# Kernel optimization log

Hardware: AMD Instinct MI355X
Metric: run time of the kernel (lower is better)

## Reference

```python
import jax, jax.numpy as jnp
import numpy as np

# dims: batch, seq_len, d_model, heads, head_dim, n_buckets
B, L, DM, H, DH, K = 4, 4096, 1024, 16, 64, 8
C = L // K            # chunk length after bucket sort (512); extra_len==0 for these dims
CS = 0.1              # cluster_score mixing weight


def setup_inputs() -> dict:
    key = jax.random.key(0)
    ks = jax.random.split(key, 12)
    s = 0.02
    def p(k, shape):
        return jax.random.normal(k, shape, jnp.float32) * s
    return {
        "inputs_q": jax.random.normal(ks[0], (B, L, DM), jnp.float32),
        "wq": p(ks[1], (DM, H, DH)), "bq": jnp.zeros((H, DH), jnp.float32),
        "wk": p(ks[2], (DM, H, DH)), "bk": jnp.zeros((H, DH), jnp.float32),
        "wv": p(ks[3], (DM, H, DH)), "bv": jnp.zeros((H, DH), jnp.float32),
        "w_shared": p(ks[4], (H, DH, K)),
        "w_qscore": p(ks[5], (H, DH, K)),
        "w_kscore": p(ks[6], (H, DH, K)),
        "wo": p(ks[7], (H, DH, DM)), "bo": jnp.zeros((DM,), jnp.float32),
    }


def reference(inputs_q, wq, bq, wk, bk, wv, bv, w_shared, w_qscore, w_kscore, wo, bo):
    scale = 1.0 / np.sqrt(DH)
    # QKV projections (DenseGeneral to (H, DH))
    q = jnp.einsum('bld,dhk->blhk', inputs_q, wq) + bq  # [B,L,H,DH]
    k = jnp.einsum('bld,dhk->blhk', inputs_q, wk) + bk
    v = jnp.einsum('bld,dhk->blhk', inputs_q, wv) + bv

    # learned linear cluster scores on stop-gradient q/k
    mix_q = (1.0 - CS) * w_shared + CS * w_qscore  # [H,DH,K]
    mix_k = (1.0 - CS) * w_shared + CS * w_kscore
    qs = jnp.einsum('blhd,hdk->blhk', jax.lax.stop_gradient(q), mix_q)  # [B,L,H,K]
    ksc = jnp.einsum('blhd,hdk->blhk', jax.lax.stop_gradient(k), mix_k)

    # bucket assignment = argmax learned score; per-(batch,head) stable sort by bucket id
    bq_id = jnp.argmax(qs, -1).transpose(0, 2, 1)   # [B,H,L]
    bk_id = jnp.argmax(ksc, -1).transpose(0, 2, 1)
    sort_q = jnp.argsort(bq_id, axis=-1)            # stable in jax
    sort_k = jnp.argsort(bk_id, axis=-1)

    qh = q.transpose(0, 2, 1, 3)  # [B,H,L,DH]
    kh = k.transpose(0, 2, 1, 3)
    vh = v.transpose(0, 2, 1, 3)
    sq = jnp.take_along_axis(qh, sort_q[..., None], axis=2).reshape(B, H, K, C, DH)
    sk = jnp.take_along_axis(kh, sort_k[..., None], axis=2).reshape(B, H, K, C, DH)
    sv = jnp.take_along_axis(vh, sort_k[..., None], axis=2).reshape(B, H, K, C, DH)

    # block attention within each bucket chunk
    logits = jnp.einsum('bhncd,bhned->bhnce', sq, sk) * scale  # [B,H,K,C,C]
    attn = jax.nn.softmax(logits, axis=-1)
    o = jnp.einsum('bhnce,bhned->bhncd', attn, sv).reshape(B, H, L, DH)

    # unsort back to original token order
    inv_q = jnp.argsort(sort_q, axis=-1)
    o = jnp.take_along_axis(o, inv_q[..., None], axis=2)  # [B,H,L,DH]
    o = o.transpose(0, 2, 1, 3)                            # [B,L,H,DH]

    out = jnp.einsum('blhd,hdo->blo', o, wo) + bo          # output projection

    # auxiliary load-balancing routing loss over buckets (extra_loss)
    p_q = jax.nn.softmax(qs, -1)
    p_k = jax.nn.softmax(ksc, -1)
    f_q = jax.nn.one_hot(jnp.argmax(qs, -1), K, dtype=qs.dtype)
    f_k = jax.nn.one_hot(jnp.argmax(ksc, -1), K, dtype=qs.dtype)
    lq = K * jnp.mean(jnp.sum(jnp.mean(f_q, 1) * jnp.mean(p_q, 1), -1))
    lk = K * jnp.mean(jnp.sum(jnp.mean(f_k, 1) * jnp.mean(p_k, 1), -1))
    extra_loss = 0.5 * (lq + lk)
    return out, extra_loss
```

## Files before the change

### kernel.cpp

```cpp
#include <hip/hip_runtime.h>
#include <hip/hip_bf16.h>

#define BB 4
#define LL 4096
#define DM 1024
#define HH 16
#define DHD 64
#define KB 8
#define BL 16384
#define FLAGCAP 131072

typedef __attribute__((ext_vector_type(8))) short short8;
typedef __attribute__((ext_vector_type(4))) short short4v;
typedef __attribute__((ext_vector_type(4))) float float4v;

#define MFMA16(A, Bx, C) __builtin_amdgcn_mfma_f32_16x16x32_bf16(A, Bx, C, 0, 0, 0)

static __device__ __forceinline__ short bf16s(float f) {
  __hip_bfloat16 h = __float2bfloat16(f);
  return *reinterpret_cast<short*>(&h);
}
static __device__ __forceinline__ float b2f(short s) {
  __hip_bfloat16 h = *reinterpret_cast<__hip_bfloat16*>(&s);
  return __bfloat162float(h);
}
static __device__ __forceinline__ void gl16(const void* g, void* l) {
  __builtin_amdgcn_global_load_lds(
      (const __attribute__((address_space(1))) void*)g,
      (__attribute__((address_space(3))) void*)l, 16, 0, 0);
}

__global__ __launch_bounds__(256) void prep_wt(const float* __restrict__ wq,
                                               const float* __restrict__ wk,
                                               const float* __restrict__ wv,
                                               const float* __restrict__ wo,
                                               __hip_bfloat16* __restrict__ wt_qkv,
                                               __hip_bfloat16* __restrict__ wt_o) {
  int blk = blockIdx.x;
  int s = blk >> 8;
  int rem = blk & 255;
  int k0 = (rem >> 4) * 64;
  int n0 = (rem & 15) * 64;
  const float* src = (s == 0) ? wq : (s == 1) ? wk : (s == 2) ? wv : wo;
  __hip_bfloat16* dst = (s < 3) ? (wt_qkv + (size_t)s * 1024 * 1024) : wt_o;
  __shared__ float ls[64][65];
  int t = threadIdx.x;
#pragma unroll
  for (int p = 0; p < 4; ++p) {
    int sid = p * 256 + t;
    int r = sid >> 4, c4 = sid & 15;
    float4 v = *reinterpret_cast<const float4*>(src + (size_t)(k0 + r) * 1024 + n0 + c4 * 4);
    ls[r][c4 * 4 + 0] = v.x; ls[r][c4 * 4 + 1] = v.y;
    ls[r][c4 * 4 + 2] = v.z; ls[r][c4 * 4 + 3] = v.w;
  }
  __syncthreads();
#pragma unroll
  for (int p = 0; p < 4; ++p) {
    int sid = p * 256 + t;
    int n = sid >> 4, kq = sid & 15;
    short4v pk;
#pragma unroll
    for (int j = 0; j < 4; ++j) pk[j] = bf16s(ls[kq * 4 + j][n]);
    *reinterpret_cast<short4v*>(dst + (size_t)(n0 + n) * 1024 + k0 + kq * 4) = pk;
  }
}

__global__ __launch_bounds__(256) void prep_wsc(const float* __restrict__ wq,
                                                const float* __restrict__ wk,
                                                const float* __restrict__ wsh,
                                                const float* __restrict__ wqs,
                                                const float* __restrict__ wks,
                                                const float* __restrict__ bq,
                                                const float* __restrict__ bk,
                                                double* __restrict__ wscg,
                                                double* __restrict__ bsc,
                                                __hip_bfloat16* __restrict__ whb,
                                                __hip_bfloat16* __restrict__ wmb) {
  int col = blockIdx.x;
  int side = col >> 7, h = (col >> 3) & 15, kk = col & 7;
  int g = side * 16 + h;
  const float* w = side ? wk : wq;
  const float* wscore = side ? wks : wqs;
  __shared__ double mix[64];
  int t = threadIdx.x;
  if (t < 64)
    mix[t] = 0.9 * (double)wsh[(h * 64 + t) * 8 + kk] +
             0.1 * (double)wscore[(h * 64 + t) * 8 + kk];
  __syncthreads();
#pragma unroll
  for (int p = 0; p < 4; ++p) {
    int d = p * 256 + t;
    double acc = 0.0;
    const float* wr = w + (size_t)d * 1024 + h * 64;
#pragma unroll
    for (int j = 0; j < 64; ++j) acc += (double)wr[j] * mix[j];
    wscg[((size_t)g * 1024 + d) * 8 + kk] = acc;
    short hi = bf16s((float)acc);
    short mid = bf16s((float)(acc - (double)b2f(hi)));
    *reinterpret_cast<short*>(whb + (size_t)col * 1024 + d) = hi;
    *reinterpret_cast<short*>(wmb + (size_t)col * 1024 + d) = mid;
  }
  if (t == 0) {
    const float* br = (side ? bk : bq) + h * 64;
    double acc = 0.0;
    for (int j = 0; j < 64; ++j) acc += (double)br[j] * mix[j];
    bsc[col] = acc;
  }
}

__global__ __launch_bounds__(256) void score_gemm(const float* __restrict__ x,
                                                  const __hip_bfloat16* __restrict__ whb,
                                                  const __hip_bfloat16* __restrict__ wmb,
                                                  const double* __restrict__ bsc,
                                                  __hip_bfloat16* __restrict__ xb,
                                                  int* __restrict__ bid,
                                                  float* __restrict__ psumg,
                                                  int* __restrict__ flagcnt,
                                                  int* __restrict__ list) {
  __shared__ char sm[81920];
  int t = threadIdx.x;
  int m0 = blockIdx.x * 64;
  int n0 = blockIdx.y * 128;
  int lane = t & 63;
  int wu = __builtin_amdgcn_readfirstlane(t >> 6);
  int lm = lane & 15, quad = lane >> 4;
  int wmr = (wu & 1) * 32, wn = (wu >> 1) * 64;
  int rb = wu * 32, rr = lane >> 3, phys = lane & 7;

  auto STAGEB = [&](int bufsel, int k0) {
    char* base = sm + 16384 + bufsel * 32768;
#pragma unroll
    for (int p = 0; p < 4; ++p) {
      int row = rb + p * 8 + rr;
      int kc = (phys - row) & 7;
      gl16(whb + (size_t)(n0 + row) * 1024 + k0 + kc * 8, base + (rb + p * 8) * 128);
      gl16(wmb + (size_t)(n0 + row) * 1024 + k0 + kc * 8, base + 16384 + (rb + p * 8) * 128);
    }
  };

  float4 xf[2][2];
  auto LOADX = [&](int k0) {
#pragma unroll
    for (int p = 0; p < 2; ++p) {
      int sid = p * 256 + t;
      int m = sid >> 3, kc = sid & 7;
      const float* ap = x + (size_t)(m0 + m) * 1024 + k0 + kc * 8;
      xf[p][0] = *reinterpret_cast<const float4*>(ap);
      xf[p][1] = *reinterpret_cast<const float4*>(ap + 4);
    }
  };

  STAGEB(0, 0);
  LOADX(0);

  float4v zero = {0.f, 0.f, 0.f, 0.f};
  float4v acc[2][4];
#pragma unroll
  for (int i = 0; i < 2; ++i)
#pragma unroll
    for (int j = 0; j < 4; ++j) acc[i][j] = zero;

#pragma unroll 1
  for (int kt = 0; kt < 16; ++kt) {
    int k0 = kt * 64;
    short8 hi[2], lo[2];
#pragma unroll
    for (int p = 0; p < 2; ++p) {
      float vv[8] = {xf[p][0].x, xf[p][0].y, xf[p][0].z, xf[p][0].w,
                     xf[p][1].x, xf[p][1].y, xf[p][1].z, xf[p][1].w};
#pragma unroll
      for (int e = 0; e < 8; ++e) {
        short h = bf16s(vv[e]);
        hi[p][e] = h;
        lo[p][e] = bf16s(vv[e] - b2f(h));
      }
    }
    asm volatile("" ::: "memory");
    __builtin_amdgcn_s_barrier();
    asm volatile("" ::: "memory");
#pragma unroll
    for (int p = 0; p < 2; ++p) {
      int sid = p * 256 + t;
      int m = sid >> 3, kc = sid & 7;
      *reinterpret_cast<short8*>(sm + m * 128 + ((kc + m) & 7) * 16) = hi[p];
      *reinterpret_cast<short8*>(sm + 8192 + m * 128 + ((kc + m) & 7) * 16) = lo[p];
      if (blockIdx.y == 0)
        *reinterpret_cast<short8*>(xb + (size_t)(m0 + m) * 1024 + k0 + kc * 8) = hi[p];
    }
    if (kt < 15) {
      STAGEB((kt + 1) & 1, k0 + 64);
      LOADX(k0 + 64);
      asm volatile("s_waitcnt vmcnt(12)" ::: "memory");
    } else {
      asm volatile("s_waitcnt vmcnt(0)" ::: "memory");
    }
    asm volatile("s_waitcnt lgkmcnt(0)" ::: "memory");
    __builtin_amdgcn_s_barrier();
    asm volatile("" ::: "memory");

    const char* bb = sm + 16384 + (kt & 1) * 32768;
#pragma unroll
    for (int kh = 0; kh < 2; ++kh) {
      short8 ah[2], al[2], bh[4], bm[4];
#pragma unroll
      for (int i = 0; i < 2; ++i) {
        int row = wmr + i * 16 + lm;
        int ph = ((kh * 4 + quad) + row) & 7;
        ah[i] = *reinterpret_cast<const short8*>(sm + row * 128 + ph * 16);
        al[i] = *reinterpret_cast<const short8*>(sm + 8192 + row * 128 + ph * 16);
      }
#pragma unroll
      for (int j = 0; j < 4; ++j) {
        int rn = wn + j * 16 + lm;
        int ph = ((kh * 4 + quad) + rn) & 7;
        bh[j] = *reinterpret_cast<const short8*>(bb + rn * 128 + ph * 16);
        bm[j] = *reinterpret_cast<const short8*>(bb + 16384 + rn * 128 + ph * 16);
      }
#pragma unroll
      for (int i = 0; i < 2; ++i)
#pragma unroll
        for (int j = 0; j < 4; ++j) {
          acc[i][j] = MFMA16(ah[i], bh[j], acc[i][j]);
          acc[i][j] = MFMA16(ah[i], bm[j], acc[i][j]);
          acc[i][j] = MFMA16(al[i], bh[j], acc[i][j]);
        }
    }
  }

  int b = m0 >> 12;
  int l0 = m0 & 4095;
  int kk = lm & 7;
#pragma unroll
  for (int j = 0; j < 4; ++j) {
    int n = n0 + wn + j * 16 + lm;
    int g = n >> 3;
    int side = g >> 4, h = g & 15;
    int slab = (side * 4 + b) * 16 + h;
    float bias = (float)bsc[n];
    float pp = 0.f;
#pragma unroll
    for (int i = 0; i < 2; ++i)
#pragma unroll
      for (int r = 0; r < 4; ++r) {
        float v = acc[i][j][r] + bias;
        float bmx = v; int bi = kk;
#pragma unroll
        for (int o = 1; o < 8; o <<= 1) {
          float vo = __shfl_xor(bmx, o);
          int io = __shfl_xor(bi, o);
          if (vo > bmx || (vo == bmx && io < bi)) { bmx = vo; bi = io; }
        }
        float vm = (kk == bi) ? -3.0e38f : v;
#pragma unroll
        for (int o = 1; o < 8; o <<= 1) vm = fmaxf(vm, __shfl_xor(vm, o));
        float e = __expf(v - bmx);
        float es = e;
#pragma unroll
        for (int o = 1; o < 8; o <<= 1) es += __shfl_xor(es, o);
        pp += e * (1.f / es);
        int l = l0 + wmr + i * 16 + quad * 4 + r;
        if (kk == 0) {
          bid[(slab << 12) | l] = bi;
          if (bmx - vm < 5e-4f) {
            int pos = atomicAdd(flagcnt, 1);
            if (pos < FLAGCAP) list[pos] = (slab << 12) | l;
          }
        }
      }
    pp += __shfl_xor(pp, 16);
    pp += __shfl_xor(pp, 32);
    if (quad == 0) atomicAdd(&psumg[slab * 8 + kk], pp);
  }
}

__global__ __launch_bounds__(256) void refine_kernel(const float* __restrict__ x,
                                                     const double* __restrict__ wscg,
                                                     const double* __restrict__ bsc,
                                                     const int* __restrict__ flagcnt,
                                                     const int* __restrict__ list,
                                                     int* __restrict__ bid) {
  int lane = threadIdx.x & 63;
  int w = threadIdx.x >> 6;
  int cnt = flagcnt[0];
  if (cnt > FLAGCAP) cnt = FLAGCAP;
  for (int i = blockIdx.x * 4 + w; i < cnt; i += 1024) {
    int e = list[i];
    int slab = e >> 12, l = e & 4095;
    int side = slab >> 6, b = (slab >> 4) & 3, h = slab & 15;
    int g = side * 16 + h;
    int row = b * 4096 + l;
    double acc[8] = {0, 0, 0, 0, 0, 0, 0, 0};
    const float* xr = x + (size_t)row * 1024 + lane * 16;
    const double* wr = wscg + ((size_t)g * 1024 + lane * 16) * 8;
#pragma unroll
    for (int dd = 0; dd < 16; ++dd) {
      double xv = (double)xr[dd];
#pragma unroll
      for (int j = 0; j < 8; ++j) acc[j] += xv * wr[dd * 8 + j];
    }
#pragma unroll
    for (int j = 0; j < 8; ++j) {
      double v = acc[j];
      v += __shfl_xor(v, 32); v += __shfl_xor(v, 16); v += __shfl_xor(v, 8);
      v += __shfl_xor(v, 4);  v += __shfl_xor(v, 2);  v += __shfl_xor(v, 1);
      acc[j] = v + bsc[g * 8 + j];
    }
    if (lane == 0) {
      double mx = acc[0]; int am = 0;
#pragma unroll
      for (int j = 1; j < 8; ++j) { if (acc[j] > mx) { mx = acc[j]; am = j; } }
      bid[(slab << 12) | l] = am;
    }
  }
}

__global__ __launch_bounds__(256) void sort_kernel(const int* __restrict__ bid,
                                                   int* __restrict__ sortq,
                                                   int* __restrict__ sortk,
                                                   int* __restrict__ cntg) {
  int blk = blockIdx.x;
  int side = blk >> 6, b = (blk >> 4) & 3, h = blk & 15;
  const int* ids = bid + (((side * 4 + b) * 16 + h) << 12);
  int* outp = (side ? sortk : sortq) + ((b * 16 + h) << 12);
  __shared__ int cnt[8][257];
  __shared__ int base[8];
  int t = threadIdx.x;
  int loc[16];
  int hist[8] = {0, 0, 0, 0, 0, 0, 0, 0};
#pragma unroll
  for (int j = 0; j < 16; ++j) { loc[j] = ids[t * 16 + j] & 7; hist[loc[j]]++; }
#pragma unroll
  for (int k = 0; k < 8; ++k) cnt[k][t + 1] = hist[k];
  if (t < 8) cnt[t][0] = 0;
  __syncthreads();
  if (t < 8) {
    for (int i = 1; i <= 256; ++i) cnt[t][i] += cnt[t][i - 1];
  }
  __syncthreads();
  if (t == 0) {
    int run = 0;
    for (int k = 0; k < 8; ++k) { base[k] = run; run += cnt[k][256]; }
  }
  if (t < 8) cntg[((side * 4 + b) * 16 + h) * 8 + t] = cnt[t][256];
  __syncthreads();
#pragma unroll
  for (int j = 0; j < 16; ++j) {
    int k = loc[j];
    int before = 0;
#pragma unroll
    for (int i = 0; i < 16; ++i) before += (i < j && loc[i] == k) ? 1 : 0;
    int pos = base[k] + cnt[k][t] + before;
    outp[pos] = t * 16 + j;
  }
}

template <bool CBF16>
__global__ __launch_bounds__(512, 2) void gemm256(const __hip_bfloat16* __restrict__ A,
                                                  const __hip_bfloat16* __restrict__ Bt,
                                                  void* __restrict__ Cv,
                                                  const float* __restrict__ b0,
                                                  const float* __restrict__ b1,
                                                  const float* __restrict__ b2,
                                                  int nblk, int cpx) {
  __shared__ char sm[131072];
  int t = threadIdx.x;
  int blk = (blockIdx.x & 7) * cpx + (blockIdx.x >> 3);
  int m0 = (blk / nblk) * 256;
  int n0 = (blk % nblk) * 256;
  int lane = t & 63;
  int wu = __builtin_amdgcn_readfirstlane(t >> 6);
  int lm = lane & 15, quad = lane >> 4;
  int rr = lane >> 3, phys = lane & 7;
  int wrow = (wu & 1) * 64;
  int wcol = (wu >> 1) * 32;

  constexpr int QM[4] = {0, 0, 1, 1};
  constexpr int QN[4] = {0, 1, 1, 0};

  auto STAGE = [&](char* bufn, int j, int kS) {
    const int mat = (j == 1 || j == 2) ? 1 : 0;
    const int hm = (j >= 2) ? 1 : 0;
    const __hip_bfloat16* src = mat ? Bt : A;
    int gb = mat ? n0 : m0;
    char* lb = bufn + mat * 32768 + hm * 16384;
#pragma unroll
    for (int i = 0; i < 2; ++i) {
      int r = hm * 128 + (wu * 2 + i) * 8 + rr;
      int kc = (phys - r) & 7;
      gl16(src + (size_t)(gb + r) * 1024 + kS + kc * 8, lb + (wu * 2 + i) * 1024);
    }
  };

#pragma unroll
  for (int j = 0; j < 4; ++j) STAGE(sm, j, 0);

  float4v zero = {0.f, 0.f, 0.f, 0.f};
  float4v acc[4][4][2];
#pragma unroll
  for (int q = 0; q < 4; ++q)
#pragma unroll
    for (int mi = 0; mi < 4; ++mi)
#pragma unroll
      for (int ni = 0; ni < 2; ++ni) acc[q][mi][ni] = zero;

  short8 a[4][2], b[2][2];
  auto READA = [&](const char* bc, int qm) {
#pragma unroll
    for (int mi = 0; mi < 4; ++mi) {
      int row = qm * 128 + wrow + mi * 16 + lm;
#pragma unroll
      for (int ks = 0; ks < 2; ++ks) {
        int ph = ((ks * 4 + quad) + row) & 7;
        a[mi][ks] = *reinterpret_cast<const short8*>(bc + row * 128 + ph * 16);
      }
    }
  };
  auto READB = [&](const char* bc, int qn) {
#pragma unroll
    for (int ni = 0; ni < 2; ++ni) {
      int rn = qn * 128 + wcol + ni * 16 + lm;
#pragma unroll
      for (int ks = 0; ks < 2; ++ks) {
        int ph = ((ks * 4 + quad) + rn) & 7;
        b[ni][ks] = *reinterpret_cast<const short8*>(bc + 32768 + rn * 128 + ph * 16);
      }
    }
  };

#pragma unroll 1
  for (int kt = 0; kt < 16; ++kt) {
    char* bc = sm + ((kt & 1) << 16);
    char* bn = sm + (((kt & 1) ^ 1) << 16);
    int kS = (kt < 15) ? (kt + 1) * 64 : 960;
#pragma unroll
    for (int j = 0; j < 4; ++j) {
      if (j < 3) {
        asm volatile("s_waitcnt vmcnt(4)" ::: "memory");
        __builtin_amdgcn_s_barrier();
      }
      if (j == 0) { READA(bc, 0); READB(bc, 0); }
      else if (j == 1) { READB(bc, 1); }
      else if (j == 2) { READA(bc, 1); }
      else { READB(bc, 0); }
      STAGE(bn, j, kS);
      __builtin_amdgcn_s_setprio(1);
#pragma unroll
      for (int mi = 0; mi < 4; ++mi)
#pragma unroll
        for (int ni = 0; ni < 2; ++ni)
#pragma unroll
          for (int ks = 0; ks < 2; ++ks)
            acc[j][mi][ni] = MFMA16(a[mi][ks], b[ni][ks], acc[j][mi][ni]);
      __builtin_amdgcn_s_setprio(0);
    }
  }
  asm volatile("s_waitcnt vmcnt(0)" ::: "memory");

  if constexpr (CBF16) {
#pragma unroll
    for (int j = 0; j < 4; ++j)
#pragma unroll
      for (int mi = 0; mi < 4; ++mi)
#pragma unroll
        for (int ni = 0; ni < 2; ++ni) {
          int nn = n0 + QN[j] * 128 + wcol + ni * 16 + lm;
          int s = nn >> 10, nnb = nn & 1023;
          const float* bias = (s == 0) ? b0 : (s == 1) ? b1 : b2;
          float bvx = bias[nnb];
          __hip_bfloat16* C = (__hip_bfloat16*)Cv + (size_t)s * BL * 1024;
#pragma unroll
          for (int r = 0; r < 4; ++r) {
            int row = m0 + QM[j] * 128 + wrow + mi * 16 + quad * 4 + r;
            C[(size_t)row * 1024 + nnb] = __float2bfloat16(acc[j][mi][ni][r] + bvx);
          }
        }
  } else {
    float* C = (float*)Cv;
#pragma unroll
    for (int j = 0; j < 4; ++j)
#pragma unroll
      for (int mi = 0; mi < 4; ++mi)
#pragma unroll
        for (int ni = 0; ni < 2; ++ni) {
          int nn = n0 + QN[j] * 128 + wcol + ni * 16 + lm;
          float bvx = b0[nn];
#pragma unroll
          for (int r = 0; r < 4; ++r) {
            int row = m0 + QM[j] * 128 + wrow + mi * 16 + quad * 4 + r;
            C[(size_t)row * 1024 + nn] = acc[j][mi][ni][r] + bvx;
          }
        }
  }
}

__global__ __launch_bounds__(256) void vt_kernel(const __hip_bfloat16* __restrict__ vb,
                                                 const int* __restrict__ sortk,
                                                 __hip_bfloat16* __restrict__ vT) {
  int cid = blockIdx.x;
  int b = cid >> 7, h = (cid >> 3) & 15, n = cid & 7;
  int sbase = ((b * 16 + h) << 12) + n * 512;
  __shared__ __hip_bfloat16 ls[64][72];
  int t = threadIdx.x;
  for (int kt = 0; kt < 8; ++kt) {
    __syncthreads();
#pragma unroll
    for (int p = 0; p < 2; ++p) {
      int sid = p * 256 + t;
      int key = sid >> 3, kc = sid & 7;
      int tok = sortk[sbase + kt * 64 + key];
      short8 v = *reinterpret_cast<const short8*>(vb + ((size_t)(b * 4096 + tok) * 16 + h) * 64 + kc * 8);
      *reinterpret_cast<short8*>(&ls[key][kc * 8]) = v;
    }
    __syncthreads();
#pragma unroll
    for (int p = 0; p < 2; ++p) {
      int sid = p * 256 + t;
      int dim = sid >> 3, kc = sid & 7;
      short8 o;
#pragma unroll
      for (int j = 0; j < 8; ++j) o[j] = *reinterpret_cast<short*>(&ls[kc * 8 + j][dim]);
      *reinterpret_cast<short8*>(vT + ((size_t)cid * 64 + dim) * 512 + kt * 64 + kc * 8) = o;
    }
  }
}

__global__ __launch_bounds__(256) void attn_kernel(const __hip_bfloat16* __restrict__ qb,
                                                   const __hip_bfloat16* __restrict__ kb,
                                                   const __hip_bfloat16* __restrict__ vT,
                                                   const int* __restrict__ sortq,
                                                   const int* __restrict__ sortk,
                                                   __hip_bfloat16* __restrict__ ao) {
  __shared__ char sm[25600];
  int t = threadIdx.x;
  int lane = t & 63, w = t >> 6;
  int lm = lane & 15, quad = lane >> 4;
  int cid = blockIdx.x >> 3, qt = blockIdx.x & 7;
  int b = cid >> 7, h = (cid >> 3) & 15, n = cid & 7;
  int sbase = (b * 16 + h) << 12;
  int psOff = 16384 + w * 2304;

  int qtok = sortq[sbase + n * 512 + qt * 64 + w * 16 + lm];
  const __hip_bfloat16* qp = qb + ((size_t)(b * 4096 + qtok) * 16 + h) * 64 + quad * 8;
  short8 aq0 = *reinterpret_cast<const short8*>(qp);
  short8 aq1 = *reinterpret_cast<const short8*>(qp + 32);

  float4v zero = {0.f, 0.f, 0.f, 0.f};
  float4v accO[4];
#pragma unroll
  for (int i = 0; i < 4; ++i) accO[i] = zero;
  float lsum[4] = {0.f, 0.f, 0.f, 0.f};

  for (int kt = 0; kt < 8; ++kt) {
    __syncthreads();
#pragma unroll
    for (int p = 0; p < 2; ++p) {
      int sid = p * 256 + t;
      int row = sid >> 3, kc = sid & 7;
      int tok = sortk[sbase + n * 512 + kt * 64 + row];
      short8 kv = *reinterpret_cast<const short8*>(kb + ((size_t)(b * 4096 + tok) * 16 + h) * 64 + kc * 8);
      *reinterpret_cast<short8*>(sm + row * 128 + ((kc + row) & 7) * 16) = kv;
      short8 vv = *reinterpret_cast<const short8*>(vT + ((size_t)cid * 64 + row) * 512 + kt * 64 + kc * 8);
      *reinterpret_cast<short8*>(sm + 8192 + row * 128 + ((kc + row) & 7) * 16) = vv;
    }
    __syncthreads();
#pragma unroll
    for (int nt = 0; nt < 4; ++nt) {
      int key = nt * 16 + lm;
      int ph0 = (quad + key) & 7;
      int ph1 = (4 + quad + key) & 7;
      short8 bk0 = *reinterpret_cast<const short8*>(sm + key * 128 + ph0 * 16);
      short8 bk1 = *reinterpret_cast<const short8*>(sm + key * 128 + ph1 * 16);
      float4v S = zero;
      S = MFMA16(aq0, bk0, S);
      S = MFMA16(aq1, bk1, S);
#pragma unroll
      for (int r = 0; r < 4; ++r) {
        float e = __expf(S[r] * 0.125f);
        lsum[r] += e;
        *reinterpret_cast<short*>(sm + psOff + (quad * 4 + r) * 144 + key * 2) = bf16s(e);
      }
    }
    __builtin_amdgcn_s_waitcnt(0);
#pragma unroll
    for (int ks = 0; ks < 2; ++ks) {
      short8 ap = *reinterpret_cast<const short8*>(sm + psOff + lm * 144 + ks * 64 + quad * 16);
#pragma unroll
      for (int dt = 0; dt < 4; ++dt) {
        int dim = dt * 16 + lm;
        int ph = (ks * 4 + quad + dim) & 7;
        short8 bv = *reinterpret_cast<const short8*>(sm + 8192 + dim * 128 + ph * 16);
        accO[dt] = MFMA16(ap, bv, accO[dt]);
      }
    }
  }
#pragma unroll
  for (int r = 0; r < 4; ++r) {
    float l = lsum[r];
    l += __shfl_xor(l, 1); l += __shfl_xor(l, 2);
    l += __shfl_xor(l, 4); l += __shfl_xor(l, 8);
    lsum[r] = 1.f / l;
  }
#pragma unroll
  for (int dt = 0; dt < 4; ++dt)
#pragma unroll
    for (int r = 0; r < 4; ++r)
      *reinterpret_cast<short*>(sm + psOff + (quad * 4 + r) * 144 + (dt * 16 + lm) * 2) =
          bf16s(accO[dt][r] * lsum[r]);
  __builtin_amdgcn_s_waitcnt(0);
  int q2 = lane >> 2, c = lane & 3;
  int tok2 = sortq[sbase + n * 512 + qt * 64 + w * 16 + q2];
  __hip_bfloat16* op = ao + ((size_t)(b * 4096 + tok2) * 16 + h) * 64;
  short8 o0 = *reinterpret_cast<const short8*>(sm + psOff + q2 * 144 + c * 16);
  short8 o1 = *reinterpret_cast<const short8*>(sm + psOff + q2 * 144 + (c + 4) * 16);
  *reinterpret_cast<short8*>(op + c * 8) = o0;
  *reinterpret_cast<short8*>(op + (c + 4) * 8) = o1;
}

__global__ __launch_bounds__(1024) void loss_kernel(const int* __restrict__ cntg,
                                                    const float* __restrict__ psumg,
                                                    float* __restrict__ out) {
  int t = threadIdx.x;
  float term = ((float)cntg[t] * (1.f / 4096.f)) * (psumg[t] * (1.f / 4096.f));
#pragma unroll
  for (int o = 1; o < 64; o <<= 1) term += __shfl_xor(term, o);
  __shared__ float wsum[16];
  if ((t & 63) == 0) wsum[t >> 6] = term;
  __syncthreads();
  if (t == 0) {
    float s = 0.f;
    for (int i = 0; i < 16; ++i) s += wsum[i];
    out[16777216] = s * (1.f / 16.f);
  }
}

extern "C" void kernel_launch(void* const* d_in, const int* in_sizes, int n_in,
                              void* d_out, int out_size, void* d_ws, size_t ws_size,
                              hipStream_t stream) {
  (void)in_sizes; (void)n_in; (void)out_size; (void)ws_size;
  const float* x   = (const float*)d_in[0];
  const float* wq  = (const float*)d_in[1];
  const float* bq  = (const float*)d_in[2];
  const float* wk  = (const float*)d_in[3];
  const float* bk  = (const float*)d_in[4];
  const float* wv  = (const float*)d_in[5];
  const float* bv  = (const float*)d_in[6];
  const float* wsh = (const float*)d_in[7];
  const float* wqs = (const float*)d_in[8];
  const float* wks = (const float*)d_in[9];
  const float* wo  = (const float*)d_in[10];
  const float* bo  = (const float*)d_in[11];

  char* ws = (char*)d_ws;
  __hip_bfloat16* wt_qkv = (__hip_bfloat16*)(ws + 0);
  __hip_bfloat16* wt_o   = (__hip_bfloat16*)(ws + 6291456);
  double* wscg  = (double*)(ws + 8388608);
  double* bsc   = (double*)(ws + 10485760);
  __hip_bfloat16* qkv  = (__hip_bfloat16*)(ws + 10487808);
  __hip_bfloat16* whb = (__hip_bfloat16*)(ws + 109051904);
  __hip_bfloat16* wmb = (__hip_bfloat16*)(ws + 109576192);
  int* flagcnt = (int*)(ws + 110100480);
  int* list    = (int*)(ws + 110100736);
  __hip_bfloat16* attn = (__hip_bfloat16*)(ws + 111151104);
  int* bid    = (int*)(ws + 144705536);
  int* sortq  = (int*)(ws + 146802688);
  int* sortk  = (int*)(ws + 147851264);
  float* psumg = (float*)(ws + 148899840);
  int* cntg    = (int*)(ws + 148903936);
  __hip_bfloat16* vT = (__hip_bfloat16*)d_out;
  __hip_bfloat16* xb = (__hip_bfloat16*)((char*)d_out + 33554432);
  float* out = (float*)d_out;

  hipMemsetAsync(psumg, 0, 8192, stream);
  hipMemsetAsync(flagcnt, 0, 4, stream);
  prep_wt<<<1024, 256, 0, stream>>>(wq, wk, wv, wo, wt_qkv, wt_o);
  prep_wsc<<<256, 256, 0, stream>>>(wq, wk, wsh, wqs, wks, bq, bk, wscg, bsc, whb, wmb);
  score_gemm<<<dim3(256, 2), 256, 0, stream>>>(x, whb, wmb, bsc, xb, bid, psumg, flagcnt, list);
  refine_kernel<<<256, 256, 0, stream>>>(x, wscg, bsc, flagcnt, list, bid);
  sort_kernel<<<128, 256, 0, stream>>>(bid, sortq, sortk, cntg);
  gemm256<true><<<768, 512, 0, stream>>>(xb, wt_qkv, qkv, bq, bk, bv, 12, 96);
  vt_kernel<<<512, 256, 0, stream>>>(qkv + (size_t)2 * BL * 1024, sortk, vT);
  attn_kernel<<<4096, 256, 0, stream>>>(qkv, qkv + (size_t)BL * 1024, vT, sortq, sortk, attn);
  gemm256<false><<<256, 512, 0, stream>>>(attn, wt_o, (void*)out, bo, bo, bo, 4, 32);
  loss_kernel<<<1, 1024, 0, stream>>>(cntg, psumg, out);
}
```

Before: 520.2 us.

## Load GEMM B operand directly from global into registers, halve LDS

The 256x256 GEMM now stages only the A tile through LDS. B fragments are loaded straight from global memory into registers in MFMA layout and double-buffered across k-steps. The quadrant order is changed so each A fragment set is reused across two B quadrants, and there is one barrier per k-iteration instead of three. LDS use is halved, but the B loads are uncoalesced 16-byte per-lane reads that rely on L2/cache hits, and register pressure rises from the extra fragment buffers.

```diff
diff --git a/kernel.cpp b/kernel.cpp
--- a/kernel.cpp
+++ b/kernel.cpp
@@ -362,7 +362,7 @@
                                                   const float* __restrict__ b1,
                                                   const float* __restrict__ b2,
                                                   int nblk, int cpx) {
-  __shared__ char sm[131072];
+  __shared__ char sm[65536];
   int t = threadIdx.x;
   int blk = (blockIdx.x & 7) * cpx + (blockIdx.x >> 3);
   int m0 = (blk / nblk) * 256;
@@ -374,25 +374,42 @@
   int wrow = (wu & 1) * 64;
   int wcol = (wu >> 1) * 32;
 
-  constexpr int QM[4] = {0, 0, 1, 1};
-  constexpr int QN[4] = {0, 1, 1, 0};
-
-  auto STAGE = [&](char* bufn, int j, int kS) {
-    const int mat = (j == 1 || j == 2) ? 1 : 0;
-    const int hm = (j >= 2) ? 1 : 0;
-    const __hip_bfloat16* src = mat ? Bt : A;
-    int gb = mat ? n0 : m0;
-    char* lb = bufn + mat * 32768 + hm * 16384;
+  constexpr int QM[4] = {0, 1, 1, 0};
+  constexpr int QN[4] = {0, 0, 1, 1};
+
+  auto STAGEA = [&](char* bufn, int hm, int kS) {
 #pragma unroll
     for (int i = 0; i < 2; ++i) {
       int r = hm * 128 + (wu * 2 + i) * 8 + rr;
       int kc = (phys - r) & 7;
-      gl16(src + (size_t)(gb + r) * 1024 + kS + kc * 8, lb + (wu * 2 + i) * 1024);
+      gl16(A + (size_t)(m0 + r) * 1024 + kS + kc * 8,
+           bufn + hm * 16384 + (wu * 2 + i) * 1024);
     }
   };
 
-#pragma unroll
-  for (int j = 0; j < 4; ++j) STAGE(sm, j, 0);
+  const __hip_bfloat16* bp[2][2][2];
+#pragma unroll
+  for (int q = 0; q < 2; ++q)
+#pragma unroll
+    for (int ni = 0; ni < 2; ++ni)
+#pragma unroll
+      for (int ks = 0; ks < 2; ++ks)
+        bp[q][ni][ks] = Bt + (size_t)(n0 + q * 128 + wcol + ni * 16 + lm) * 1024 +
+                        ks * 32 + quad * 8;
+
+  short8 b0f[2][2], b1f[2][2];
+  auto LOADB = [&](short8 (&bb)[2][2], int q, int kS) {
+#pragma unroll
+    for (int ni = 0; ni < 2; ++ni)
+#pragma unroll
+      for (int ks = 0; ks < 2; ++ks)
+        bb[ni][ks] = *reinterpret_cast<const short8*>(bp[q][ni][ks] + kS);
+  };
+
+  STAGEA(sm, 0, 0);
+  STAGEA(sm, 1, 0);
+  LOADB(b0f, 0, 0);
+  LOADB(b1f, 1, 0);
 
   float4v zero = {0.f, 0.f, 0.f, 0.f};
   float4v acc[4][4][2];
@@ -403,56 +420,48 @@
 #pragma unroll
       for (int ni = 0; ni < 2; ++ni) acc[q][mi][ni] = zero;
 
-  short8 a[4][2], b[2][2];
-  auto READA = [&](const char* bc, int qm) {
+  short8 a0[4][2], a1[4][2];
+  auto READA = [&](short8 (&aa)[4][2], const char* bc, int qm) {
 #pragma unroll
     for (int mi = 0; mi < 4; ++mi) {
       int row = qm * 128 + wrow + mi * 16 + lm;
 #pragma unroll
       for (int ks = 0; ks < 2; ++ks) {
         int ph = ((ks * 4 + quad) + row) & 7;
-        a[mi][ks] = *reinterpret_cast<const short8*>(bc + row * 128 + ph * 16);
+        aa[mi][ks] = *reinterpret_cast<const short8*>(bc + row * 128 + ph * 16);
       }
     }
   };
-  auto READB = [&](const char* bc, int qn) {
-#pragma unroll
-    for (int ni = 0; ni < 2; ++ni) {
-      int rn = qn * 128 + wcol + ni * 16 + lm;
-#pragma unroll
-      for (int ks = 0; ks < 2; ++ks) {
-        int ph = ((ks * 4 + quad) + rn) & 7;
-        b[ni][ks] = *reinterpret_cast<const short8*>(bc + 32768 + rn * 128 + ph * 16);
-      }
-    }
-  };
+
+#define QMFMA(J, AA, BB)                                                     \
+  __builtin_amdgcn_s_setprio(1);                                             \
+  _Pragma("unroll") for (int mi = 0; mi < 4; ++mi)                           \
+      _Pragma("unroll") for (int ni = 0; ni < 2; ++ni)                       \
+          _Pragma("unroll") for (int ks = 0; ks < 2; ++ks)                   \
+              acc[J][mi][ni] = MFMA16(AA[mi][ks], BB[ni][ks], acc[J][mi][ni]); \
+  __builtin_amdgcn_s_setprio(0);
+
+  asm volatile("s_waitcnt vmcnt(8)" ::: "memory");
+  __builtin_amdgcn_s_barrier();
 
 #pragma unroll 1
   for (int kt = 0; kt < 16; ++kt) {
-    char* bc = sm + ((kt & 1) << 16);
-    char* bn = sm + (((kt & 1) ^ 1) << 16);
+    char* bc = sm + ((kt & 1) << 15);
+    char* bn = sm + (((kt & 1) ^ 1) << 15);
     int kS = (kt < 15) ? (kt + 1) * 64 : 960;
-#pragma unroll
-    for (int j = 0; j < 4; ++j) {
-      if (j < 3) {
-        asm volatile("s_waitcnt vmcnt(4)" ::: "memory");
-        __builtin_amdgcn_s_barrier();
-      }
-      if (j == 0) { READA(bc, 0); READB(bc, 0); }
-      else if (j == 1) { READB(bc, 1); }
-      else if (j == 2) { READA(bc, 1); }
-      else { READB(bc, 0); }
-      STAGE(bn, j, kS);
-      __builtin_amdgcn_s_setprio(1);
-#pragma unroll
-      for (int mi = 0; mi < 4; ++mi)
-#pragma unroll
-        for (int ni = 0; ni < 2; ++ni)
-#pragma unroll
-          for (int ks = 0; ks < 2; ++ks)
-            acc[j][mi][ni] = MFMA16(a[mi][ks], b[ni][ks], acc[j][mi][ni]);
-      __builtin_amdgcn_s_setprio(0);
-    }
+
+    READA(a0, bc, 0);
+    STAGEA(bn, 0, kS);
+    QMFMA(0, a0, b0f)
+    READA(a1, bc, 1);
+    STAGEA(bn, 1, kS);
+    QMFMA(1, a1, b0f)
+    LOADB(b0f, 0, kS);
+    QMFMA(2, a1, b1f)
+    QMFMA(3, a0, b1f)
+    LOADB(b1f, 1, kS);
+    asm volatile("s_waitcnt vmcnt(8)" ::: "memory");
+    __builtin_amdgcn_s_barrier();
   }
   asm volatile("s_waitcnt vmcnt(0)" ::: "memory");
 
@@ -491,6 +500,7 @@
           }
         }
   }
+#undef QMFMA
 }
 
 __global__ __launch_bounds__(256) void vt_kernel(const __hip_bfloat16* __restrict__ vb,
```

New measurement: 578.3 us. +11.2%, slower.

## Stage whole bucket chunk K/V in LDS once per block, loop over query tiles

Applied to the files above, without the earlier changes.

The attention kernel now launches one 512-thread block per bucket chunk instead of eight 256-thread blocks per chunk. Each block loads all 512 keys and the transposed values of its chunk into about 146 KB of LDS once, then processes four rounds of 128 queries against them. This removes the eightfold redundant gather of K/V and the per-tile barriers of the old streaming loop. In exchange, LDS use limits residency to one block (8 waves) per CU, the grid shrinks to 512 blocks, and no load overlaps compute, so latency hiding may suffer.

```diff
diff --git a/kernel.cpp b/kernel.cpp
--- a/kernel.cpp
+++ b/kernel.cpp
@@ -524,96 +524,106 @@
   }
 }
 
-__global__ __launch_bounds__(256) void attn_kernel(const __hip_bfloat16* __restrict__ qb,
-                                                   const __hip_bfloat16* __restrict__ kb,
-                                                   const __hip_bfloat16* __restrict__ vT,
-                                                   const int* __restrict__ sortq,
-                                                   const int* __restrict__ sortk,
-                                                   __hip_bfloat16* __restrict__ ao) {
-  __shared__ char sm[25600];
+__global__ __launch_bounds__(512, 2) void attn_kernel(const __hip_bfloat16* __restrict__ qb,
+                                                      const __hip_bfloat16* __restrict__ kb,
+                                                      const __hip_bfloat16* __restrict__ vT,
+                                                      const int* __restrict__ sortq,
+                                                      const int* __restrict__ sortk,
+                                                      __hip_bfloat16* __restrict__ ao) {
+  __shared__ char sm[149504];
   int t = threadIdx.x;
   int lane = t & 63, w = t >> 6;
   int lm = lane & 15, quad = lane >> 4;
-  int cid = blockIdx.x >> 3, qt = blockIdx.x & 7;
+  int cid = blockIdx.x;
   int b = cid >> 7, h = (cid >> 3) & 15, n = cid & 7;
   int sbase = (b * 16 + h) << 12;
-  int psOff = 16384 + w * 2304;
-
-  int qtok = sortq[sbase + n * 512 + qt * 64 + w * 16 + lm];
-  const __hip_bfloat16* qp = qb + ((size_t)(b * 4096 + qtok) * 16 + h) * 64 + quad * 8;
-  short8 aq0 = *reinterpret_cast<const short8*>(qp);
-  short8 aq1 = *reinterpret_cast<const short8*>(qp + 32);
+  int psOff = 131072 + w * 2304;
+
+  {
+    int row = t >> 3, kc = t & 7;
+    int sw = ((kc + row) & 7) * 16;
+#pragma unroll
+    for (int kt = 0; kt < 8; ++kt) {
+      int tok = sortk[sbase + n * 512 + kt * 64 + row];
+      short8 kv = *reinterpret_cast<const short8*>(
+          kb + ((size_t)(b * 4096 + tok) * 16 + h) * 64 + kc * 8);
+      *reinterpret_cast<short8*>(sm + kt * 8192 + row * 128 + sw) = kv;
+      short8 vv = *reinterpret_cast<const short8*>(
+          vT + ((size_t)cid * 64 + row) * 512 + kt * 64 + kc * 8);
+      *reinterpret_cast<short8*>(sm + 65536 + kt * 8192 + row * 128 + sw) = vv;
+    }
+  }
+  __syncthreads();
 
   float4v zero = {0.f, 0.f, 0.f, 0.f};
-  float4v accO[4];
-#pragma unroll
-  for (int i = 0; i < 4; ++i) accO[i] = zero;
-  float lsum[4] = {0.f, 0.f, 0.f, 0.f};
-
-  for (int kt = 0; kt < 8; ++kt) {
-    __syncthreads();
-#pragma unroll
-    for (int p = 0; p < 2; ++p) {
-      int sid = p * 256 + t;
-      int row = sid >> 3, kc = sid & 7;
-      int tok = sortk[sbase + n * 512 + kt * 64 + row];
-      short8 kv = *reinterpret_cast<const short8*>(kb + ((size_t)(b * 4096 + tok) * 16 + h) * 64 + kc * 8);
-      *reinterpret_cast<short8*>(sm + row * 128 + ((kc + row) & 7) * 16) = kv;
-      short8 vv = *reinterpret_cast<const short8*>(vT + ((size_t)cid * 64 + row) * 512 + kt * 64 + kc * 8);
-      *reinterpret_cast<short8*>(sm + 8192 + row * 128 + ((kc + row) & 7) * 16) = vv;
-    }
-    __syncthreads();
-#pragma unroll
-    for (int nt = 0; nt < 4; ++nt) {
-      int key = nt * 16 + lm;
-      int ph0 = (quad + key) & 7;
-      int ph1 = (4 + quad + key) & 7;
-      short8 bk0 = *reinterpret_cast<const short8*>(sm + key * 128 + ph0 * 16);
-      short8 bk1 = *reinterpret_cast<const short8*>(sm + key * 128 + ph1 * 16);
-      float4v S = zero;
-      S = MFMA16(aq0, bk0, S);
-      S = MFMA16(aq1, bk1, S);
-#pragma unroll
-      for (int r = 0; r < 4; ++r) {
-        float e = __expf(S[r] * 0.125f);
-        lsum[r] += e;
-        *reinterpret_cast<short*>(sm + psOff + (quad * 4 + r) * 144 + key * 2) = bf16s(e);
-      }
-    }
+#pragma unroll 1
+  for (int qr = 0; qr < 4; ++qr) {
+    int qtok = sortq[sbase + n * 512 + qr * 128 + w * 16 + lm];
+    const __hip_bfloat16* qp = qb + ((size_t)(b * 4096 + qtok) * 16 + h) * 64 + quad * 8;
+    short8 aq0 = *reinterpret_cast<const short8*>(qp);
+    short8 aq1 = *reinterpret_cast<const short8*>(qp + 32);
+
+    float4v accO[4];
+#pragma unroll
+    for (int i = 0; i < 4; ++i) accO[i] = zero;
+    float lsum[4] = {0.f, 0.f, 0.f, 0.f};
+
+#pragma unroll 1
+    for (int kt = 0; kt < 8; ++kt) {
+      const char* Kt = sm + kt * 8192;
+      const char* Vt = sm + 65536 + kt * 8192;
+#pragma unroll
+      for (int nt = 0; nt < 4; ++nt) {
+        int key = nt * 16 + lm;
+        int ph0 = (quad + key) & 7;
+        int ph1 = (4 + quad + key) & 7;
+        short8 bk0 = *reinterpret_cast<const short8*>(Kt + key * 128 + ph0 * 16);
+        short8 bk1 = *reinterpret_cast<const short8*>(Kt + key * 128 + ph1 * 16);
+        float4v S = zero;
+        S = MFMA16(aq0, bk0, S);
+        S = MFMA16(aq1, bk1, S);
+#pragma unroll
+        for (int r = 0; r < 4; ++r) {
+          float e = __expf(S[r] * 0.125f);
+          lsum[r] += e;
+          *reinterpret_cast<short*>(sm + psOff + (quad * 4 + r) * 144 + key * 2) = bf16s(e);
+        }
+      }
+      __builtin_amdgcn_s_waitcnt(0);
+#pragma unroll
+      for (int ks = 0; ks < 2; ++ks) {
+        short8 ap = *reinterpret_cast<const short8*>(sm + psOff + lm * 144 + ks * 64 + quad * 16);
+#pragma unroll
+        for (int dt = 0; dt < 4; ++dt) {
+          int dim = dt * 16 + lm;
+          int ph = (ks * 4 + quad + dim) & 7;
+          short8 bv = *reinterpret_cast<const short8*>(Vt + dim * 128 + ph * 16);
+          accO[dt] = MFMA16(ap, bv, accO[dt]);
+        }
+      }
+    }
+#pragma unroll
+    for (int r = 0; r < 4; ++r) {
+      float l = lsum[r];
+      l += __shfl_xor(l, 1); l += __shfl_xor(l, 2);
+      l += __shfl_xor(l, 4); l += __shfl_xor(l, 8);
+      lsum[r] = 1.f / l;
+    }
+#pragma unroll
+    for (int dt = 0; dt < 4; ++dt)
+#pragma unroll
+      for (int r = 0; r < 4; ++r)
+        *reinterpret_cast<short*>(sm + psOff + (quad * 4 + r) * 144 + (dt * 16 + lm) * 2) =
+            bf16s(accO[dt][r] * lsum[r]);
     __builtin_amdgcn_s_waitcnt(0);
-#pragma unroll
-    for (int ks = 0; ks < 2; ++ks) {
-      short8 ap = *reinterpret_cast<const short8*>(sm + psOff + lm * 144 + ks * 64 + quad * 16);
-#pragma unroll
-      for (int dt = 0; dt < 4; ++dt) {
-        int dim = dt * 16 + lm;
-        int ph = (ks * 4 + quad + dim) & 7;
-        short8 bv = *reinterpret_cast<const short8*>(sm + 8192 + dim * 128 + ph * 16);
-        accO[dt] = MFMA16(ap, bv, accO[dt]);
-      }
-    }
-  }
-#pragma unroll
-  for (int r = 0; r < 4; ++r) {
-    float l = lsum[r];
-    l += __shfl_xor(l, 1); l += __shfl_xor(l, 2);
-    l += __shfl_xor(l, 4); l += __shfl_xor(l, 8);
-    lsum[r] = 1.f / l;
-  }
-#pragma unroll
-  for (int dt = 0; dt < 4; ++dt)
-#pragma unroll
-    for (int r = 0; r < 4; ++r)
-      *reinterpret_cast<short*>(sm + psOff + (quad * 4 + r) * 144 + (dt * 16 + lm) * 2) =
-          bf16s(accO[dt][r] * lsum[r]);
-  __builtin_amdgcn_s_waitcnt(0);
-  int q2 = lane >> 2, c = lane & 3;
-  int tok2 = sortq[sbase + n * 512 + qt * 64 + w * 16 + q2];
-  __hip_bfloat16* op = ao + ((size_t)(b * 4096 + tok2) * 16 + h) * 64;
-  short8 o0 = *reinterpret_cast<const short8*>(sm + psOff + q2 * 144 + c * 16);
-  short8 o1 = *reinterpret_cast<const short8*>(sm + psOff + q2 * 144 + (c + 4) * 16);
-  *reinterpret_cast<short8*>(op + c * 8) = o0;
-  *reinterpret_cast<short8*>(op + (c + 4) * 8) = o1;
+    int q2 = lane >> 2, c = lane & 3;
+    int tok2 = sortq[sbase + n * 512 + qr * 128 + w * 16 + q2];
+    __hip_bfloat16* op = ao + ((size_t)(b * 4096 + tok2) * 16 + h) * 64;
+    short8 o0 = *reinterpret_cast<const short8*>(sm + psOff + q2 * 144 + c * 16);
+    short8 o1 = *reinterpret_cast<const short8*>(sm + psOff + q2 * 144 + (c + 4) * 16);
+    *reinterpret_cast<short8*>(op + c * 8) = o0;
+    *reinterpret_cast<short8*>(op + (c + 4) * 8) = o1;
+  }
 }
 
 __global__ __launch_bounds__(1024) void loss_kernel(const int* __restrict__ cntg,
@@ -679,7 +689,7 @@
   sort_kernel<<<128, 256, 0, stream>>>(bid, sortq, sortk, cntg);
   gemm256<true><<<768, 512, 0, stream>>>(xb, wt_qkv, qkv, bq, bk, bv, 12, 96);
   vt_kernel<<<512, 256, 0, stream>>>(qkv + (size_t)2 * BL * 1024, sortk, vT);
-  attn_kernel<<<4096, 256, 0, stream>>>(qkv, qkv + (size_t)BL * 1024, vT, sortq, sortk, attn);
+  attn_kernel<<<512, 512, 0, stream>>>(qkv, qkv + (size_t)BL * 1024, vT, sortq, sortk, attn);
   gemm256<false><<<256, 512, 0, stream>>>(attn, wt_o, (void*)out, bo, bo, bo, 4, 32);
   loss_kernel<<<1, 1024, 0, stream>>>(cntg, psumg, out);
 }
```

After: 515.3 us. Within noise of the previous version (-0.9%).
